# Optimization experiments

Measured on AMD Instinct MI355X. Metric: run time of the kernel, lower is better.

The kernel has to match this reference:

```python
import jax, jax.numpy as jnp
import numpy as np

D = 384      # ViT-S feature dim (feat_dim_lookup['s'])
H = 6        # module forces num_heads = 6
L = 12       # ViT-S depth
RATIO = 0.1  # attention_mask_ratio
EPS = 1e-6


def layernorm(x, g, b):
    m = x.mean(-1, keepdims=True)
    v = ((x - m) ** 2).mean(-1, keepdims=True)
    return (x - m) * jax.lax.rsqrt(v + EPS) * g + b


def masked_attn(x, w_qkv, b_qkv, w_o, b_o):
    # Patch._fix_attn_masking: full softmax attention, threshold at ratio*row_max, renormalize.
    B, N, Dm = x.shape
    dh = Dm // H
    qkv = (x @ w_qkv + b_qkv).reshape(B, N, 3, H, dh)
    q = qkv[:, :, 0].transpose(0, 2, 1, 3)  # [B,H,N,dh]
    k = qkv[:, :, 1].transpose(0, 2, 1, 3)
    v = qkv[:, :, 2].transpose(0, 2, 1, 3)
    scores = jnp.einsum('bhqd,bhkd->bhqk', q, k) * (dh ** -0.5)
    attn = jax.nn.softmax(scores, axis=-1)
    thresh = RATIO * attn.max(axis=-1, keepdims=True)
    attn = jnp.where(attn >= thresh, attn, 0.0)
    attn = attn / attn.sum(axis=-1, keepdims=True)  # re-normalize
    out = jnp.einsum('bhqk,bhkd->bhqd', attn, v)
    out = out.transpose(0, 2, 1, 3).reshape(B, N, Dm)
    return out @ w_o + b_o, attn


def block(x, p):
    w_qkv, b_qkv, w_o, b_o, g1, be1, g2, be2, w1, b1, w2, b2 = p
    h, attn = masked_attn(layernorm(x, g1, be1), w_qkv, b_qkv, w_o, b_o)
    x = x + h
    h = layernorm(x, g2, be2) @ w1 + b1
    h = jax.nn.gelu(h, approximate=False) @ w2 + b2
    return x + h, attn


def setup_inputs() -> dict:
    key = jax.random.key(0)
    ks = jax.random.split(key, 8)
    B, N = 2, 962  # 2 transforms; (1+(160-8)//5)**2 + 1 cls = 962 tokens
    s = 0.02
    return {
        'x': jax.random.normal(ks[0], (B, N, D), jnp.float32),
        'w_qkv': jax.random.normal(ks[1], (L, D, 3 * D), jnp.float32) * s,
        'b_qkv': jnp.zeros((L, 3 * D), jnp.float32),
        'w_proj': jax.random.normal(ks[2], (L, D, D), jnp.float32) * s,
        'b_proj': jnp.zeros((L, D), jnp.float32),
        'ln1_g': jnp.ones((L, D), jnp.float32),
        'ln1_b': jnp.zeros((L, D), jnp.float32),
        'ln2_g': jnp.ones((L, D), jnp.float32),
        'ln2_b': jnp.zeros((L, D), jnp.float32),
        'w_fc1': jax.random.normal(ks[3], (L, D, 4 * D), jnp.float32) * s,
        'b_fc1': jnp.zeros((L, 4 * D), jnp.float32),
        'w_fc2': jax.random.normal(ks[4], (L, 4 * D, D), jnp.float32) * s,
        'b_fc2': jnp.zeros((L, D), jnp.float32),
        'lnf_g': jnp.ones((D,), jnp.float32),
        'lnf_b': jnp.zeros((D,), jnp.float32),
    }


def reference(x, w_qkv, b_qkv, w_proj, b_proj, ln1_g, ln1_b, ln2_g, ln2_b,
              w_fc1, b_fc1, w_fc2, b_fc2, lnf_g, lnf_b):
    params = (w_qkv, b_qkv, w_proj, b_proj, ln1_g, ln1_b, ln2_g, ln2_b,
              w_fc1, b_fc1, w_fc2, b_fc2)
    first = jax.tree_util.tree_map(lambda a: a[:-1], params)
    last = jax.tree_util.tree_map(lambda a: a[-1], params)

    def scan_fn(h, p):
        h, _ = block(h, p)
        return h, None

    x, _ = jax.lax.scan(scan_fn, x, first)  # blocks 0..L-2
    x, attn = block(x, last)                # last block, keep masked attention
    feats = layernorm(x, lnf_g, lnf_b)      # [B, N, D]
    return feats, attn
```

## Files before the change

### kernel.cpp

```cpp
#include <hip/hip_runtime.h>
#include <hip/hip_bf16.h>
#include <math.h>

typedef __bf16 bf16_t;
typedef __bf16 bf16x8 __attribute__((ext_vector_type(8)));
typedef float f32x4 __attribute__((ext_vector_type(4)));

#define LN10 2.302585092994046f

__global__ void __launch_bounds__(256) tr_k(
    const float* __restrict__ W, bf16_t* __restrict__ Wt, int K, int N)
{
    __shared__ float T[32][33];
    const size_t per = (size_t)K * N;
    const float* Wl = W + blockIdx.z * per;
    bf16_t* Wtl = Wt + blockIdx.z * per;
    int n0 = blockIdx.x * 32, k0 = blockIdx.y * 32;
    int tx = threadIdx.x & 31, ty = threadIdx.x >> 5;
#pragma unroll
    for (int i = 0; i < 4; ++i)
        T[ty + 8 * i][tx] = Wl[(size_t)(k0 + ty + 8 * i) * N + n0 + tx];
    __syncthreads();
#pragma unroll
    for (int i = 0; i < 4; ++i)
        Wtl[(size_t)(n0 + ty + 8 * i) * K + k0 + tx] = (bf16_t)T[tx][ty + 8 * i];
}

template <int MODE>
__global__ void __launch_bounds__(256) gemm_k(
    const bf16_t* __restrict__ A, const bf16_t* __restrict__ Bt,
    const float* __restrict__ bias, int M, int N, int K,
    float* __restrict__ resid, bf16_t* __restrict__ outb,
    bf16_t* __restrict__ qb, bf16_t* __restrict__ kb, bf16_t* __restrict__ vtb)
{
    __shared__ alignas(16) bf16_t As[2][64][72];
    __shared__ alignas(16) bf16_t Bs[2][64][72];

    const int tid  = threadIdx.x;
    const int wave = tid >> 6, lane = tid & 63;
    const int m0 = blockIdx.y * 64, n0 = blockIdx.x * 64;
    const int rb = (wave >> 1) * 32, cb = (wave & 1) * 32;
    const int q4 = lane >> 4, mm = lane & 15;

    const int lrow = tid >> 3;
    const int lcol = (tid & 7) * 8;

    const bf16_t* pA0 = A  + (size_t)(m0 + lrow) * K + lcol;
    const bf16_t* pA1 = pA0 + (size_t)32 * K;
    const bf16_t* pB0 = Bt + (size_t)(n0 + lrow) * K + lcol;
    const bf16_t* pB1 = pB0 + (size_t)32 * K;

    f32x4 acc[2][2] = {};
    bf16x8 va0, va1, vb0, vb1;

    va0 = *(const bf16x8*)(pA0);
    va1 = *(const bf16x8*)(pA1);
    vb0 = *(const bf16x8*)(pB0);
    vb1 = *(const bf16x8*)(pB1);
    *(bf16x8*)(&As[0][lrow][lcol])      = va0;
    *(bf16x8*)(&As[0][lrow + 32][lcol]) = va1;
    *(bf16x8*)(&Bs[0][lrow][lcol])      = vb0;
    *(bf16x8*)(&Bs[0][lrow + 32][lcol]) = vb1;

    int cur = 0;
    for (int k0 = 0; k0 < K; k0 += 64) {
        __syncthreads();
        const bool has_next = (k0 + 64 < K);
        if (has_next) {
            va0 = *(const bf16x8*)(pA0 + k0 + 64);
            va1 = *(const bf16x8*)(pA1 + k0 + 64);
            vb0 = *(const bf16x8*)(pB0 + k0 + 64);
            vb1 = *(const bf16x8*)(pB1 + k0 + 64);
        }
#pragma unroll
        for (int kc = 0; kc < 64; kc += 32) {
            bf16x8 a0 = *(const bf16x8*)(&As[cur][rb + mm][kc + q4 * 8]);
            bf16x8 a1 = *(const bf16x8*)(&As[cur][rb + 16 + mm][kc + q4 * 8]);
            bf16x8 b0 = *(const bf16x8*)(&Bs[cur][cb + mm][kc + q4 * 8]);
            bf16x8 b1 = *(const bf16x8*)(&Bs[cur][cb + 16 + mm][kc + q4 * 8]);
            acc[0][0] = __builtin_amdgcn_mfma_f32_16x16x32_bf16(a0, b0, acc[0][0], 0, 0, 0);
            acc[0][1] = __builtin_amdgcn_mfma_f32_16x16x32_bf16(a0, b1, acc[0][1], 0, 0, 0);
            acc[1][0] = __builtin_amdgcn_mfma_f32_16x16x32_bf16(a1, b0, acc[1][0], 0, 0, 0);
            acc[1][1] = __builtin_amdgcn_mfma_f32_16x16x32_bf16(a1, b1, acc[1][1], 0, 0, 0);
        }
        if (has_next) {
            int nxt = cur ^ 1;
            *(bf16x8*)(&As[nxt][lrow][lcol])      = va0;
            *(bf16x8*)(&As[nxt][lrow + 32][lcol]) = va1;
            *(bf16x8*)(&Bs[nxt][lrow][lcol])      = vb0;
            *(bf16x8*)(&Bs[nxt][lrow + 32][lcol]) = vb1;
            cur = nxt;
        }
    }

#pragma unroll
    for (int i = 0; i < 2; ++i)
#pragma unroll
    for (int j = 0; j < 2; ++j) {
        int gc = n0 + cb + j * 16 + mm;
        float bv = bias[gc];
#pragma unroll
        for (int r = 0; r < 4; ++r) {
            int gr = m0 + rb + i * 16 + q4 * 4 + r;
            if (gr >= M) continue;
            float val = acc[i][j][r] + bv;
            if (MODE == 1) {
                resid[(size_t)gr * N + gc] += val;
            } else if (MODE == 2) {
                float g = 0.5f * val * (1.0f + erff(val * 0.70710678118654752f));
                outb[(size_t)gr * N + gc] = (bf16_t)g;
            } else {
                int which = gc / 384, rem = gc % 384;
                int h = rem >> 6, d = rem & 63;
                int b = gr / 962, n = gr % 962;
                int bh = b * 6 + h;
                bf16_t bvv = (bf16_t)val;
                if (which == 0)      qb[((size_t)bh * 962 + n) * 64 + d] = bvv;
                else if (which == 1) kb[((size_t)bh * 962 + n) * 64 + d] = bvv;
                else                 vtb[((size_t)bh * 64 + d) * 992 + n] = bvv;
            }
        }
    }
}

__global__ void __launch_bounds__(256) attn_k(
    const bf16_t* __restrict__ qb, const bf16_t* __restrict__ kb,
    const bf16_t* __restrict__ vtb, bf16_t* __restrict__ attnout,
    float* __restrict__ attn_save)
{
    __shared__ alignas(16) bf16_t S[16][1000];

    const int tid  = threadIdx.x;
    const int wave = tid >> 6, lane = tid & 63;
    const int q4 = lane >> 4, mm = lane & 15;
    const int bh = blockIdx.y, qt = blockIdx.x;
    const int qrow0 = qt * 16;

    int qr = qrow0 + mm; if (qr > 961) qr = 961;
    const bf16_t* qptr = qb + ((size_t)bh * 962 + qr) * 64 + q4 * 8;
    bf16x8 aq0 = *(const bf16x8*)(qptr);
    bf16x8 aq1 = *(const bf16x8*)(qptr + 32);

    for (int ct = wave; ct < 61; ct += 4) {
        int kr = ct * 16 + mm; if (kr > 961) kr = 961;
        const bf16_t* kptr = kb + ((size_t)bh * 962 + kr) * 64 + q4 * 8;
        bf16x8 b0 = *(const bf16x8*)(kptr);
        bf16x8 b1 = *(const bf16x8*)(kptr + 32);
        f32x4 acc = {};
        acc = __builtin_amdgcn_mfma_f32_16x16x32_bf16(aq0, b0, acc, 0, 0, 0);
        acc = __builtin_amdgcn_mfma_f32_16x16x32_bf16(aq1, b1, acc, 0, 0, 0);
        int col = ct * 16 + mm;
#pragma unroll
        for (int r = 0; r < 4; ++r) {
            int row = q4 * 4 + r;
            if (col < 962) S[row][col] = (bf16_t)(acc[r] * 0.125f);
        }
    }
    __syncthreads();

    const int trow = tid >> 4, ti = tid & 15;
    float mx = -1e30f;
    for (int c = ti; c < 962; c += 16) mx = fmaxf(mx, (float)S[trow][c]);
#pragma unroll
    for (int off = 8; off > 0; off >>= 1) mx = fmaxf(mx, __shfl_xor(mx, off, 16));
    float thr = mx - LN10;
    float sum = 0.f;
    for (int c = ti; c < 962; c += 16) {
        float v = (float)S[trow][c];
        if (v >= thr) sum += __expf(v - mx);
    }
#pragma unroll
    for (int off = 8; off > 0; off >>= 1) sum += __shfl_xor(sum, off, 16);
    float inv = 1.0f / sum;

    int row_g = qrow0 + trow;
    for (int c = ti; c < 1000; c += 16) {
        float p = 0.f;
        if (c < 962) {
            float v = (float)S[trow][c];
            p = (v >= thr) ? __expf(v - mx) * inv : 0.f;
        }
        S[trow][c] = (bf16_t)p;
        if (attn_save && c < 962 && row_g < 962)
            attn_save[((size_t)bh * 962 + row_g) * 962 + c] = p;
    }
    __syncthreads();

    const int wc0 = wave * 16;
    f32x4 o = {};
    for (int kc = 0; kc < 31; ++kc) {
        bf16x8 pa = *(const bf16x8*)(&S[mm][kc * 32 + q4 * 8]);
        bf16x8 vb = *(const bf16x8*)(vtb + ((size_t)bh * 64 + wc0 + mm) * 992 + kc * 32 + q4 * 8);
        o = __builtin_amdgcn_mfma_f32_16x16x32_bf16(pa, vb, o, 0, 0, 0);
    }
    int b = bh / 6, h = bh % 6;
#pragma unroll
    for (int r = 0; r < 4; ++r) {
        int qrr = qrow0 + q4 * 4 + r;
        if (qrr < 962)
            attnout[((size_t)(b * 962 + qrr)) * 384 + h * 64 + wc0 + mm] = (bf16_t)o[r];
    }
}

template <typename OT>
__global__ void __launch_bounds__(256) ln_k(
    const float* __restrict__ x, const float* __restrict__ g,
    const float* __restrict__ b, OT* __restrict__ out)
{
    int t = blockIdx.x * 4 + (threadIdx.x >> 6);
    int lane = threadIdx.x & 63;
    const float* xp = x + (size_t)t * 384;
    float v[6];
    float s = 0.f;
#pragma unroll
    for (int i = 0; i < 6; ++i) { v[i] = xp[lane + 64 * i]; s += v[i]; }
    for (int off = 32; off > 0; off >>= 1) s += __shfl_xor(s, off);
    float mean = s * (1.0f / 384.0f);
    float s2 = 0.f;
#pragma unroll
    for (int i = 0; i < 6; ++i) { float d = v[i] - mean; s2 += d * d; }
    for (int off = 32; off > 0; off >>= 1) s2 += __shfl_xor(s2, off);
    float rstd = rsqrtf(s2 * (1.0f / 384.0f) + 1e-6f);
#pragma unroll
    for (int i = 0; i < 6; ++i) {
        int c = lane + 64 * i;
        float y = (v[i] - mean) * rstd * g[c] + b[c];
        out[(size_t)t * 384 + c] = (OT)y;
    }
}

extern "C" void kernel_launch(void* const* d_in, const int* in_sizes, int n_in,
                              void* d_out, int out_size, void* d_ws, size_t ws_size,
                              hipStream_t stream)
{
    const float* xin    = (const float*)d_in[0];
    const float* w_qkv  = (const float*)d_in[1];
    const float* b_qkv  = (const float*)d_in[2];
    const float* w_proj = (const float*)d_in[3];
    const float* b_proj = (const float*)d_in[4];
    const float* ln1g   = (const float*)d_in[5];
    const float* ln1b   = (const float*)d_in[6];
    const float* ln2g   = (const float*)d_in[7];
    const float* ln2b   = (const float*)d_in[8];
    const float* w_fc1  = (const float*)d_in[9];
    const float* b_fc1  = (const float*)d_in[10];
    const float* w_fc2  = (const float*)d_in[11];
    const float* b_fc2  = (const float*)d_in[12];
    const float* lnfg   = (const float*)d_in[13];
    const float* lnfb   = (const float*)d_in[14];

    float* feats     = (float*)d_out;
    float* attn_save = feats + 738816;

    char* p = (char*)d_ws;
    auto alloc = [&](size_t bytes) {
        char* r = p;
        p += (bytes + 255) & ~(size_t)255;
        return r;
    };
    float*  x_f32   = (float*)alloc(1924ull * 384 * 4);
    bf16_t* xn      = (bf16_t*)alloc(1984ull * 384 * 2);
    bf16_t* qbuf    = (bf16_t*)alloc(12ull * 962 * 64 * 2);
    bf16_t* kbuf    = (bf16_t*)alloc(12ull * 962 * 64 * 2);
    bf16_t* vtbuf   = (bf16_t*)alloc(12ull * 64 * 992 * 2);
    bf16_t* attnout = (bf16_t*)alloc(1984ull * 384 * 2);
    bf16_t* mlp1    = (bf16_t*)alloc(1984ull * 1536 * 2);
    bf16_t* wt_qkv  = (bf16_t*)alloc(12ull * 1152 * 384 * 2);
    bf16_t* wt_proj = (bf16_t*)alloc(12ull * 384 * 384 * 2);
    bf16_t* wt_fc1  = (bf16_t*)alloc(12ull * 1536 * 384 * 2);
    bf16_t* wt_fc2  = (bf16_t*)alloc(12ull * 384 * 1536 * 2);

    tr_k<<<dim3(36, 12, 12), dim3(256), 0, stream>>>(w_qkv,  wt_qkv,  384, 1152);
    tr_k<<<dim3(12, 12, 12), dim3(256), 0, stream>>>(w_proj, wt_proj, 384, 384);
    tr_k<<<dim3(48, 12, 12), dim3(256), 0, stream>>>(w_fc1,  wt_fc1,  384, 1536);
    tr_k<<<dim3(12, 48, 12), dim3(256), 0, stream>>>(w_fc2,  wt_fc2,  1536, 384);

    hipMemcpyAsync(x_f32, xin, 738816ull * 4, hipMemcpyDeviceToDevice, stream);

    for (int l = 0; l < 12; ++l) {
        ln_k<bf16_t><<<dim3(481), dim3(256), 0, stream>>>(x_f32, ln1g + l * 384, ln1b + l * 384, xn);
        gemm_k<0><<<dim3(18, 31), dim3(256), 0, stream>>>(
            xn, wt_qkv + (size_t)l * 1152 * 384, b_qkv + l * 1152,
            1924, 1152, 384, nullptr, nullptr, qbuf, kbuf, vtbuf);
        attn_k<<<dim3(61, 12), dim3(256), 0, stream>>>(
            qbuf, kbuf, vtbuf, attnout, (l == 11) ? attn_save : (float*)nullptr);
        gemm_k<1><<<dim3(6, 31), dim3(256), 0, stream>>>(
            attnout, wt_proj + (size_t)l * 384 * 384, b_proj + l * 384,
            1924, 384, 384, x_f32, nullptr, nullptr, nullptr, nullptr);
        ln_k<bf16_t><<<dim3(481), dim3(256), 0, stream>>>(x_f32, ln2g + l * 384, ln2b + l * 384, xn);
        gemm_k<2><<<dim3(24, 31), dim3(256), 0, stream>>>(
            xn, wt_fc1 + (size_t)l * 1536 * 384, b_fc1 + l * 1536,
            1924, 1536, 384, nullptr, mlp1, nullptr, nullptr, nullptr);
        gemm_k<1><<<dim3(6, 31), dim3(256), 0, stream>>>(
            mlp1, wt_fc2 + (size_t)l * 384 * 1536, b_fc2 + l * 384,
            1924, 384, 1536, x_f32, nullptr, nullptr, nullptr, nullptr);
    }
    ln_k<float><<<dim3(481), dim3(256), 0, stream>>>(x_f32, lnfg, lnfb, feats);
}
```

Before: 1.183 ms.

## Drop LDS staging in GEMMs, split-K with atomics, register-resident attention softmax

The GEMM kernel stops staging tiles through double-buffered shared memory. Each wave now loads its MFMA operands straight from global memory through a fully unrolled, compile-time-length K loop. The proj and fc2 GEMMs use split-K (2 and 4 slices) with atomicAdd into the residual, so more blocks are in flight, at the cost of atomic traffic and non-deterministic summation order. The attention softmax keeps each row chunk in registers with vectorised LDS reads and writes. It thresholds on exp(v-mx) >= 0.1 and pads the tail columns with a large negative value, removing the repeated passes over shared memory.

```diff
diff --git a/kernel.cpp b/kernel.cpp
--- a/kernel.cpp
+++ b/kernel.cpp
@@ -6,7 +6,7 @@
 typedef __bf16 bf16x8 __attribute__((ext_vector_type(8)));
 typedef float f32x4 __attribute__((ext_vector_type(4)));
 
-#define LN10 2.302585092994046f
+#define NEGBIG -3.0e38f
 
 __global__ void __launch_bounds__(256) tr_k(
     const float* __restrict__ W, bf16_t* __restrict__ Wt, int K, int N)
@@ -26,71 +26,37 @@
         Wtl[(size_t)(n0 + ty + 8 * i) * K + k0 + tx] = (bf16_t)T[tx][ty + 8 * i];
 }
 
-template <int MODE>
-__global__ void __launch_bounds__(256) gemm_k(
-    const bf16_t* __restrict__ A, const bf16_t* __restrict__ Bt,
-    const float* __restrict__ bias, int M, int N, int K,
+template <int MODE, int KLEN, int SPLIT>
+__global__ void __launch_bounds__(256) gemm_nl(
+    const bf16_t* __restrict__ A, int lda,
+    const bf16_t* __restrict__ Bt, int ldb,
+    const float* __restrict__ bias, int M, int N,
     float* __restrict__ resid, bf16_t* __restrict__ outb,
     bf16_t* __restrict__ qb, bf16_t* __restrict__ kb, bf16_t* __restrict__ vtb)
 {
-    __shared__ alignas(16) bf16_t As[2][64][72];
-    __shared__ alignas(16) bf16_t Bs[2][64][72];
-
     const int tid  = threadIdx.x;
     const int wave = tid >> 6, lane = tid & 63;
     const int m0 = blockIdx.y * 64, n0 = blockIdx.x * 64;
     const int rb = (wave >> 1) * 32, cb = (wave & 1) * 32;
     const int q4 = lane >> 4, mm = lane & 15;
-
-    const int lrow = tid >> 3;
-    const int lcol = (tid & 7) * 8;
-
-    const bf16_t* pA0 = A  + (size_t)(m0 + lrow) * K + lcol;
-    const bf16_t* pA1 = pA0 + (size_t)32 * K;
-    const bf16_t* pB0 = Bt + (size_t)(n0 + lrow) * K + lcol;
-    const bf16_t* pB1 = pB0 + (size_t)32 * K;
+    const int ks = (SPLIT > 1) ? blockIdx.z * KLEN : 0;
+
+    const bf16_t* pa0 = A  + (size_t)(m0 + rb + mm) * lda + ks + q4 * 8;
+    const bf16_t* pa1 = pa0 + (size_t)16 * lda;
+    const bf16_t* pb0 = Bt + (size_t)(n0 + cb + mm) * ldb + ks + q4 * 8;
+    const bf16_t* pb1 = pb0 + (size_t)16 * ldb;
 
     f32x4 acc[2][2] = {};
-    bf16x8 va0, va1, vb0, vb1;
-
-    va0 = *(const bf16x8*)(pA0);
-    va1 = *(const bf16x8*)(pA1);
-    vb0 = *(const bf16x8*)(pB0);
-    vb1 = *(const bf16x8*)(pB1);
-    *(bf16x8*)(&As[0][lrow][lcol])      = va0;
-    *(bf16x8*)(&As[0][lrow + 32][lcol]) = va1;
-    *(bf16x8*)(&Bs[0][lrow][lcol])      = vb0;
-    *(bf16x8*)(&Bs[0][lrow + 32][lcol]) = vb1;
-
-    int cur = 0;
-    for (int k0 = 0; k0 < K; k0 += 64) {
-        __syncthreads();
-        const bool has_next = (k0 + 64 < K);
-        if (has_next) {
-            va0 = *(const bf16x8*)(pA0 + k0 + 64);
-            va1 = *(const bf16x8*)(pA1 + k0 + 64);
-            vb0 = *(const bf16x8*)(pB0 + k0 + 64);
-            vb1 = *(const bf16x8*)(pB1 + k0 + 64);
-        }
-#pragma unroll
-        for (int kc = 0; kc < 64; kc += 32) {
-            bf16x8 a0 = *(const bf16x8*)(&As[cur][rb + mm][kc + q4 * 8]);
-            bf16x8 a1 = *(const bf16x8*)(&As[cur][rb + 16 + mm][kc + q4 * 8]);
-            bf16x8 b0 = *(const bf16x8*)(&Bs[cur][cb + mm][kc + q4 * 8]);
-            bf16x8 b1 = *(const bf16x8*)(&Bs[cur][cb + 16 + mm][kc + q4 * 8]);
-            acc[0][0] = __builtin_amdgcn_mfma_f32_16x16x32_bf16(a0, b0, acc[0][0], 0, 0, 0);
-            acc[0][1] = __builtin_amdgcn_mfma_f32_16x16x32_bf16(a0, b1, acc[0][1], 0, 0, 0);
-            acc[1][0] = __builtin_amdgcn_mfma_f32_16x16x32_bf16(a1, b0, acc[1][0], 0, 0, 0);
-            acc[1][1] = __builtin_amdgcn_mfma_f32_16x16x32_bf16(a1, b1, acc[1][1], 0, 0, 0);
-        }
-        if (has_next) {
-            int nxt = cur ^ 1;
-            *(bf16x8*)(&As[nxt][lrow][lcol])      = va0;
-            *(bf16x8*)(&As[nxt][lrow + 32][lcol]) = va1;
-            *(bf16x8*)(&Bs[nxt][lrow][lcol])      = vb0;
-            *(bf16x8*)(&Bs[nxt][lrow + 32][lcol]) = vb1;
-            cur = nxt;
-        }
+#pragma unroll
+    for (int k = 0; k < KLEN; k += 32) {
+        bf16x8 a0 = *(const bf16x8*)(pa0 + k);
+        bf16x8 a1 = *(const bf16x8*)(pa1 + k);
+        bf16x8 b0 = *(const bf16x8*)(pb0 + k);
+        bf16x8 b1 = *(const bf16x8*)(pb1 + k);
+        acc[0][0] = __builtin_amdgcn_mfma_f32_16x16x32_bf16(a0, b0, acc[0][0], 0, 0, 0);
+        acc[0][1] = __builtin_amdgcn_mfma_f32_16x16x32_bf16(a0, b1, acc[0][1], 0, 0, 0);
+        acc[1][0] = __builtin_amdgcn_mfma_f32_16x16x32_bf16(a1, b0, acc[1][0], 0, 0, 0);
+        acc[1][1] = __builtin_amdgcn_mfma_f32_16x16x32_bf16(a1, b1, acc[1][1], 0, 0, 0);
     }
 
 #pragma unroll
@@ -98,14 +64,15 @@
 #pragma unroll
     for (int j = 0; j < 2; ++j) {
         int gc = n0 + cb + j * 16 + mm;
-        float bv = bias[gc];
+        float bv = (SPLIT == 1 || blockIdx.z == 0) ? bias[gc] : 0.f;
 #pragma unroll
         for (int r = 0; r < 4; ++r) {
             int gr = m0 + rb + i * 16 + q4 * 4 + r;
             if (gr >= M) continue;
             float val = acc[i][j][r] + bv;
             if (MODE == 1) {
-                resid[(size_t)gr * N + gc] += val;
+                if (SPLIT > 1) atomicAdd(&resid[(size_t)gr * N + gc], val);
+                else           resid[(size_t)gr * N + gc] += val;
             } else if (MODE == 2) {
                 float g = 0.5f * val * (1.0f + erff(val * 0.70710678118654752f));
                 outb[(size_t)gr * N + gc] = (bf16_t)g;
@@ -156,33 +123,62 @@
             if (col < 962) S[row][col] = (bf16_t)(acc[r] * 0.125f);
         }
     }
+    for (int idx = tid; idx < 16 * 38; idx += 256) {
+        int r = idx / 38, c = 962 + idx % 38;
+        S[r][c] = (bf16_t)NEGBIG;
+    }
     __syncthreads();
 
     const int trow = tid >> 4, ti = tid & 15;
-    float mx = -1e30f;
-    for (int c = ti; c < 962; c += 16) mx = fmaxf(mx, (float)S[trow][c]);
+    float e[8][8];
+    float mx = NEGBIG;
+#pragma unroll
+    for (int t = 0; t < 8; ++t) {
+        int c8 = ti * 8 + 128 * t;
+        bf16x8 xv;
+        if (c8 < 1000) xv = *(const bf16x8*)(&S[trow][c8]);
+        else {
+#pragma unroll
+            for (int j = 0; j < 8; ++j) xv[j] = (bf16_t)NEGBIG;
+        }
+#pragma unroll
+        for (int j = 0; j < 8; ++j) { e[t][j] = (float)xv[j]; mx = fmaxf(mx, e[t][j]); }
+    }
 #pragma unroll
     for (int off = 8; off > 0; off >>= 1) mx = fmaxf(mx, __shfl_xor(mx, off, 16));
-    float thr = mx - LN10;
+
     float sum = 0.f;
-    for (int c = ti; c < 962; c += 16) {
-        float v = (float)S[trow][c];
-        if (v >= thr) sum += __expf(v - mx);
+#pragma unroll
+    for (int t = 0; t < 8; ++t)
+#pragma unroll
+    for (int j = 0; j < 8; ++j) {
+        float ev = __expf(e[t][j] - mx);
+        e[t][j] = ev;
+        if (ev >= 0.1f) sum += ev;
     }
 #pragma unroll
     for (int off = 8; off > 0; off >>= 1) sum += __shfl_xor(sum, off, 16);
     float inv = 1.0f / sum;
 
     int row_g = qrow0 + trow;
-    for (int c = ti; c < 1000; c += 16) {
-        float p = 0.f;
-        if (c < 962) {
-            float v = (float)S[trow][c];
-            p = (v >= thr) ? __expf(v - mx) * inv : 0.f;
-        }
-        S[trow][c] = (bf16_t)p;
-        if (attn_save && c < 962 && row_g < 962)
-            attn_save[((size_t)bh * 962 + row_g) * 962 + c] = p;
+#pragma unroll
+    for (int t = 0; t < 8; ++t) {
+        int c8 = ti * 8 + 128 * t;
+        if (c8 >= 1000) continue;
+        bf16x8 pv;
+#pragma unroll
+        for (int j = 0; j < 8; ++j) {
+            float pp = (e[t][j] >= 0.1f) ? e[t][j] * inv : 0.f;
+            e[t][j] = pp;
+            pv[j] = (bf16_t)pp;
+        }
+        *(bf16x8*)(&S[trow][c8]) = pv;
+        if (attn_save && row_g < 962) {
+#pragma unroll
+            for (int j = 0; j < 8; ++j)
+                if (c8 + j < 962)
+                    attn_save[((size_t)bh * 962 + row_g) * 962 + c8 + j] = e[t][j];
+        }
     }
     __syncthreads();
 
@@ -279,21 +275,21 @@
 
     for (int l = 0; l < 12; ++l) {
         ln_k<bf16_t><<<dim3(481), dim3(256), 0, stream>>>(x_f32, ln1g + l * 384, ln1b + l * 384, xn);
-        gemm_k<0><<<dim3(18, 31), dim3(256), 0, stream>>>(
-            xn, wt_qkv + (size_t)l * 1152 * 384, b_qkv + l * 1152,
-            1924, 1152, 384, nullptr, nullptr, qbuf, kbuf, vtbuf);
+        gemm_nl<0, 384, 1><<<dim3(18, 31, 1), dim3(256), 0, stream>>>(
+            xn, 384, wt_qkv + (size_t)l * 1152 * 384, 384, b_qkv + l * 1152,
+            1924, 1152, nullptr, nullptr, qbuf, kbuf, vtbuf);
         attn_k<<<dim3(61, 12), dim3(256), 0, stream>>>(
             qbuf, kbuf, vtbuf, attnout, (l == 11) ? attn_save : (float*)nullptr);
-        gemm_k<1><<<dim3(6, 31), dim3(256), 0, stream>>>(
-            attnout, wt_proj + (size_t)l * 384 * 384, b_proj + l * 384,
-            1924, 384, 384, x_f32, nullptr, nullptr, nullptr, nullptr);
+        gemm_nl<1, 192, 2><<<dim3(6, 31, 2), dim3(256), 0, stream>>>(
+            attnout, 384, wt_proj + (size_t)l * 384 * 384, 384, b_proj + l * 384,
+            1924, 384, x_f32, nullptr, nullptr, nullptr, nullptr);
         ln_k<bf16_t><<<dim3(481), dim3(256), 0, stream>>>(x_f32, ln2g + l * 384, ln2b + l * 384, xn);
-        gemm_k<2><<<dim3(24, 31), dim3(256), 0, stream>>>(
-            xn, wt_fc1 + (size_t)l * 1536 * 384, b_fc1 + l * 1536,
-            1924, 1536, 384, nullptr, mlp1, nullptr, nullptr, nullptr);
-        gemm_k<1><<<dim3(6, 31), dim3(256), 0, stream>>>(
-            mlp1, wt_fc2 + (size_t)l * 384 * 1536, b_fc2 + l * 384,
-            1924, 384, 1536, x_f32, nullptr, nullptr, nullptr, nullptr);
+        gemm_nl<2, 384, 1><<<dim3(24, 31, 1), dim3(256), 0, stream>>>(
+            xn, 384, wt_fc1 + (size_t)l * 1536 * 384, 384, b_fc1 + l * 1536,
+            1924, 1536, nullptr, mlp1, nullptr, nullptr, nullptr);
+        gemm_nl<1, 384, 4><<<dim3(6, 31, 4), dim3(256), 0, stream>>>(
+            mlp1, 1536, wt_fc2 + (size_t)l * 384 * 1536, 1536, b_fc2 + l * 384,
+            1924, 384, x_f32, nullptr, nullptr, nullptr, nullptr);
     }
     ln_k<float><<<dim3(481), dim3(256), 0, stream>>>(x_f32, lnfg, lnfb, feats);
 }
```

After: 1.461 ms. 23.5% more time.
